# Optimization experiments

Measured on AMD Instinct MI355X. Metric: run time of the kernel, lower is better.

## Reference

```python
import jax, jax.numpy as jnp
import numpy as np

B, T, V, H = 4, 512, 8000, 7


def setup_inputs() -> dict:
    key = jax.random.key(0)
    k1, k2, k3 = jax.random.split(key, 3)
    return {
        "input_ids": jax.random.randint(k1, (B, T), 0, V),
        "frequencies": jax.random.normal(k2, (V,), dtype=jnp.float32) * 3.0,
        "amplitudes": 1.0 + jax.random.normal(k3, (V,), dtype=jnp.float32) * 0.1,
        "decay": jnp.asarray(1.5, dtype=jnp.float32),
        "chunk_size": 16,
    }


def reference(input_ids, frequencies, amplitudes, decay, chunk_size):
    h = jnp.arange(1, H + 1, dtype=frequencies.dtype)  # (H,)
    # harmonic expansion: freqs = f*[1..H], amps = A/[1..H]^decay
    all_f = frequencies[:, None] * h                    # (V, H)
    all_A = amplitudes[:, None] / h ** decay            # (V, H)
    seq_f = frequencies[input_ids][..., None] * h       # (B, T, H)
    seq_A = amplitudes[input_ids][..., None] / h ** decay

    nc = T // chunk_size
    sfc = seq_f.reshape(B, nc, chunk_size, H).transpose(1, 0, 2, 3)  # (nc,B,c,H)
    sAc = seq_A.reshape(B, nc, chunk_size, H).transpose(1, 0, 2, 3)

    def per_chunk(args):
        sf, sA = args  # (B,c,H)
        df = sf[:, :, :, None, None] - all_f[None, None, None, :, :]   # (B,c,H,V,H)
        amp = sA[:, :, :, None, None] * all_A[None, None, None, :, :]
        return 2.0 * (amp * jnp.sinc(2.0 * df)).sum(axis=(2, 4))       # (B,c,V)

    Cc = jax.lax.map(per_chunk, (sfc, sAc))            # (nc, B, c, V)
    C = Cc.transpose(1, 0, 2, 3).reshape(B, T, V)      # (B, T, V)

    cum = jnp.cumsum(C, axis=1)
    # logits[t] uses history 0..t-1 -> shift right by one, position 0 gets zeros
    logits = jnp.concatenate([jnp.zeros_like(cum[:, :1]), cum[:, :-1]], axis=1)
    return logits
```

## Files before the change

kernel.cpp:

```cpp
#include <hip/hip_runtime.h>
#include <math.h>


typedef float v2f __attribute__((ext_vector_type(2)));

constexpr int cB = 4, cT = 512, cV = 8000, cH = 7;
constexpr int GT = 4;
constexpr int NPLANE = 28;

__device__ __forceinline__ v2f pk_add(v2f a, v2f b) {
    v2f d; asm("v_pk_add_f32 %0, %1, %2" : "=v"(d) : "v"(a), "v"(b)); return d;
}
__device__ __forceinline__ v2f pk_mul(v2f a, v2f b) {
    v2f d; asm("v_pk_mul_f32 %0, %1, %2" : "=v"(d) : "v"(a), "v"(b)); return d;
}
__device__ __forceinline__ v2f pk_fma(v2f a, v2f b, v2f c) {
    v2f d; asm("v_pk_fma_f32 %0, %1, %2, %3" : "=v"(d) : "v"(a), "v"(b), "v"(c));
    return d;
}

__global__ __launch_bounds__(256) void wavelm_tab(
    const float* __restrict__ freq, const float* __restrict__ amp,
    const float* __restrict__ decay_p, float* __restrict__ tab)
{
    const int v = blockIdx.x * 256 + threadIdx.x;
    if (v >= cV) return;
    const float decay = decay_p[0];
    const float f = freq[v], A = amp[v];
    const float p2 = __builtin_amdgcn_exp2f(-decay);
    const float p3 = __builtin_amdgcn_exp2f(-decay * 1.5849625007f);
    const float p5 = __builtin_amdgcn_exp2f(-decay * 2.3219280949f);
    const float p7 = __builtin_amdgcn_exp2f(-decay * 2.8073549221f);
    const float rp[7] = {1.f, p2, p3, p2*p2, p5, p2*p3, p7};
    const float xr = f - rintf(f);
    const float s1 = __builtin_amdgcn_sinf(xr);
    const float c1 = __builtin_amdgcn_cosf(xr);
    float s = s1, c = c1;
#pragma unroll
    for (int k = 0; k < cH; ++k) {
        if (k) { const float sp = s, cp = c;
                 s = fmaf(sp, c1,  cp * s1);
                 c = fmaf(cp, c1, -(sp * s1)); }
        tab[(size_t)k * cV + v]        = s;
        tab[(size_t)(7 + k) * cV + v]  = c;
        tab[(size_t)(14 + k) * cV + v] = A * rp[k];
        tab[(size_t)(21 + k) * cV + v] = f * (float)(k + 1);
    }
}

__global__ __launch_bounds__(256) void wavelm_g(
    const int* __restrict__ ids, const float* __restrict__ tab,
    float* __restrict__ out)
{
    const int bt0 = blockIdx.y * GT;
    const int vh  = blockIdx.x * 256 + threadIdx.x;
    const bool valid = (vh * 2 < cV);
    const int vc = valid ? vh : 0;

    const v2f* tp = (const v2f*)tab;
    v2f nb[cH], sBw[cH], cBw[cH];
#pragma unroll
    for (int j = 0; j < cH; ++j) {
        const v2f s = tp[(size_t)j * (cV/2) + vc];
        const v2f c = tp[(size_t)(7 + j) * (cV/2) + vc];
        const v2f w = tp[(size_t)(14 + j) * (cV/2) + vc];
        const v2f a = tp[(size_t)(21 + j) * (cV/2) + vc];
        const v2f ws = w * 0.15915494309189535f;
        sBw[j] = s * ws;
        cBw[j] = c * ws;
        nb[j].x = -a.x;  nb[j].y = -a.y;
    }

    for (int g = 0; g < GT; ++g) {
        const int bt = bt0 + g;
        const int id = ids[bt];
        float sA[cH], cA[cH], wA[cH], aU[cH];
#pragma unroll
        for (int i = 0; i < cH; ++i) {
            sA[i] = tab[(size_t)i * cV + id];
            cA[i] = tab[(size_t)(7 + i) * cV + id];
            wA[i] = tab[(size_t)(14 + i) * cV + id];
            aU[i] = tab[(size_t)(21 + i) * cV + id];
        }

        float accx = 0.f, accy = 0.f;
        float mn = 3.0e38f, mx = 0.0f;
#pragma unroll
        for (int i = 0; i < cH; ++i) {
            v2f ai;  ai.x = aU[i];  ai.y = aU[i];
            v2f d[cH], p[cH];
#pragma unroll
            for (int j = 0; j < cH; ++j) d[j] = pk_add(ai, nb[j]);
            p[0] = d[0];
#pragma unroll
            for (int j = 1; j < cH; ++j) p[j] = pk_mul(p[j-1], d[j]);
            const float ptot = p[6].x * p[6].y;
            mn = fminf(mn, fminf(fabsf(p[6].x), fabsf(p[6].y)));
            mn = fminf(mn, fabsf(ptot));
            mx = fmaxf(mx, fabsf(ptot));
            const float rt = __builtin_amdgcn_rcpf(ptot);
            v2f r;  r.x = rt * p[6].y;  r.y = rt * p[6].x;
            v2f accS = (v2f)0.f, accC = (v2f)0.f;
#pragma unroll
            for (int j = cH - 1; j >= 1; --j) {
                const v2f inv = pk_mul(r, p[j-1]);
                accS = pk_fma(cBw[j], inv, accS);
                accC = pk_fma(sBw[j], inv, accC);
                r = pk_mul(r, d[j]);
            }
            accS = pk_fma(cBw[0], r, accS);
            accC = pk_fma(sBw[0], r, accC);
            const float tx = fmaf(sA[i], accS.x, -(cA[i] * accC.x));
            const float ty = fmaf(sA[i], accS.y, -(cA[i] * accC.y));
            accx = fmaf(wA[i], tx, accx);
            accy = fmaf(wA[i], ty, accy);
        }

        if (mn < 1e-37f || mx > 1e37f) {
            accx = 0.f;  accy = 0.f;
#pragma unroll
            for (int i = 0; i < cH; ++i) {
                float ax = 0.f, ay = 0.f;
#pragma unroll
                for (int j = 0; j < cH; ++j) {
                    const v2f w = tp[(size_t)(14 + j) * (cV/2) + vc];
                    const float dx = aU[i] + nb[j].x;
                    const float dy = aU[i] + nb[j].y;
                    const float snx = fmaf(sA[i], cBw[j].x, -(cA[i] * sBw[j].x));
                    const float sny = fmaf(sA[i], cBw[j].y, -(cA[i] * sBw[j].y));
                    float qx = snx * __builtin_amdgcn_rcpf(dx);
                    float qy = sny * __builtin_amdgcn_rcpf(dy);
                    qx = (dx == 0.f) ? w.x : qx;
                    qy = (dy == 0.f) ? w.y : qy;
                    ax += qx;  ay += qy;
                }
                accx = fmaf(wA[i], ax, accx);
                accy = fmaf(wA[i], ay, accy);
            }
        }

        if (valid) {
            v2f res;  res.x = 2.f * accx;  res.y = 2.f * accy;
            *(v2f*)(out + (size_t)bt * cV + (size_t)vh * 2) = res;
        }
    }
}

__global__ __launch_bounds__(256) void wavelm_seg(
    const float* __restrict__ out, float* __restrict__ segsum,
    int lgseg, int seglen)
{
    const int v = blockIdx.x * 256 + threadIdx.x;
    if (v >= cV) return;
    const int bs = blockIdx.y;
    const int b = bs >> lgseg, seg = bs & ((1 << lgseg) - 1);
    const float* p = out + ((size_t)b * cT + (size_t)seg * seglen) * cV + v;
    float a0 = 0.f, a1 = 0.f, a2 = 0.f, a3 = 0.f;
    for (int k = 0; k < seglen; k += 4) {
        a0 += p[(size_t)(k+0) * cV];
        a1 += p[(size_t)(k+1) * cV];
        a2 += p[(size_t)(k+2) * cV];
        a3 += p[(size_t)(k+3) * cV];
    }
    segsum[(size_t)bs * cV + v] = (a0 + a1) + (a2 + a3);
}

__global__ __launch_bounds__(256) void wavelm_scan2(
    float* __restrict__ out, const float* __restrict__ segsum,
    int lgseg, int seglen)
{
    const int v = blockIdx.x * 256 + threadIdx.x;
    if (v >= cV) return;
    const int bs = blockIdx.y;
    const int b = bs >> lgseg, seg = bs & ((1 << lgseg) - 1);
    const int nseg = 1 << lgseg;
    float base = 0.f;
    for (int sp = 0; sp < seg; ++sp)
        base += segsum[(size_t)(b * nseg + sp) * cV + v];
    float* p = out + ((size_t)b * cT + (size_t)seg * seglen) * cV + v;
    float acc = base;
#pragma unroll 8
    for (int k = 0; k < seglen; ++k) {
        const float c = p[(size_t)k * cV];
        p[(size_t)k * cV] = acc;
        acc += c;
    }
}

__global__ __launch_bounds__(256) void wavelm_scan(float* __restrict__ out)
{
    const int g = blockIdx.x * blockDim.x + threadIdx.x;
    if (g >= cB * cV) return;
    const int b = g / cV;
    const int v = g - b * cV;
    float* p = out + (size_t)b * cT * cV + v;
    float acc = 0.f;
#pragma unroll 8
    for (int t = 0; t < cT; ++t) {
        const float c = p[(size_t)t * cV];
        p[(size_t)t * cV] = acc;
        acc += c;
    }
}

extern "C" void kernel_launch(void* const* d_in, const int* in_sizes, int n_in,
                              void* d_out, int out_size, void* d_ws, size_t ws_size,
                              hipStream_t stream)
{
    const int*   ids  = (const int*)d_in[0];
    const float* freq = (const float*)d_in[1];
    const float* amp  = (const float*)d_in[2];
    const float* dec  = (const float*)d_in[3];
    float* out = (float*)d_out;
    float* tab = (float*)d_ws;
    float* segsum = tab + (size_t)NPLANE * cV;

    const size_t tab_b = (size_t)NPLANE * cV * sizeof(float);
    int lgseg = 4;
    while (lgseg > 0 &&
           tab_b + ((size_t)cB << lgseg) * cV * sizeof(float) > ws_size)
        --lgseg;
    const int use_seg =
        (lgseg > 0 &&
         tab_b + ((size_t)cB << lgseg) * cV * sizeof(float) <= ws_size) ? 1 : 0;

    wavelm_tab<<<(cV + 255) / 256, 256, 0, stream>>>(freq, amp, dec, tab);

    dim3 grid((cV / 2 + 255) / 256, cB * cT / GT);
    wavelm_g<<<grid, dim3(256), 0, stream>>>(ids, tab, out);

    if (use_seg) {
        const int nseg = 1 << lgseg;
        const int seglen = cT / nseg;
        dim3 sg((cV + 255) / 256, cB * nseg);
        wavelm_seg<<<sg, dim3(256), 0, stream>>>(out, segsum, lgseg, seglen);
        wavelm_scan2<<<sg, dim3(256), 0, stream>>>(out, segsum, lgseg, seglen);
    } else {
        const int nchains = cB * cV;
        wavelm_scan<<<(nchains + 255) / 256, dim3(256), 0, stream>>>(out);
    }
}
```

Baseline: 225.1 us.

## Fuse segment sums into main kernel and precompute packed per-token tables

The main kernel now sums its GT=8 output rows per column into a partial-sum buffer. A small scan over 64 segments and a short per-group rescan then replace the separate segment-sum pass that re-read the whole output. The table kernel also precomputes negated frequencies, scaled sin/cos terms and duplicated packed per-token values (including the 2x and sign folding), which cuts per-row loads and scalar ops in the inner loop. The fallback path now also triggers on non-finite accumulators. The cost is a larger workspace and a dependence on ws_size being big enough for the fast path.

```diff
diff --git a/kernel.cpp b/kernel.cpp
--- a/kernel.cpp
+++ b/kernel.cpp
@@ -5,8 +5,10 @@
 typedef float v2f __attribute__((ext_vector_type(2)));
 
 constexpr int cB = 4, cT = 512, cV = 8000, cH = 7;
-constexpr int GT = 4;
-constexpr int NPLANE = 28;
+constexpr int GT = 8;
+constexpr int NSEG = 64;
+constexpr int TABP  = 49;
+constexpr int TABUP = 21;
 
 __device__ __forceinline__ v2f pk_add(v2f a, v2f b) {
     v2f d; asm("v_pk_add_f32 %0, %1, %2" : "=v"(d) : "v"(a), "v"(b)); return d;
@@ -14,14 +16,17 @@
 __device__ __forceinline__ v2f pk_mul(v2f a, v2f b) {
     v2f d; asm("v_pk_mul_f32 %0, %1, %2" : "=v"(d) : "v"(a), "v"(b)); return d;
 }
-__device__ __forceinline__ v2f pk_fma(v2f a, v2f b, v2f c) {
-    v2f d; asm("v_pk_fma_f32 %0, %1, %2, %3" : "=v"(d) : "v"(a), "v"(b), "v"(c));
-    return d;
+__device__ __forceinline__ void pk_mul_ip(v2f& a, v2f b) {
+    asm("v_pk_mul_f32 %0, %0, %1" : "+v"(a) : "v"(b));
+}
+__device__ __forceinline__ void pk_acc(v2f& acc, v2f a, v2f b) {
+    asm("v_pk_fma_f32 %0, %1, %2, %0" : "+v"(acc) : "v"(a), "v"(b));
 }
 
 __global__ __launch_bounds__(256) void wavelm_tab(
     const float* __restrict__ freq, const float* __restrict__ amp,
-    const float* __restrict__ decay_p, float* __restrict__ tab)
+    const float* __restrict__ decay_p, float* __restrict__ tab,
+    v2f* __restrict__ tabU)
 {
     const int v = blockIdx.x * 256 + threadIdx.x;
     if (v >= cV) return;
@@ -32,6 +37,8 @@
     const float p5 = __builtin_amdgcn_exp2f(-decay * 2.3219280949f);
     const float p7 = __builtin_amdgcn_exp2f(-decay * 2.8073549221f);
     const float rp[7] = {1.f, p2, p3, p2*p2, p5, p2*p3, p7};
+    const float INV2PI = 0.15915494309189535f;
+
     const float xr = f - rintf(f);
     const float s1 = __builtin_amdgcn_sinf(xr);
     const float c1 = __builtin_amdgcn_cosf(xr);
@@ -41,16 +48,28 @@
         if (k) { const float sp = s, cp = c;
                  s = fmaf(sp, c1,  cp * s1);
                  c = fmaf(cp, c1, -(sp * s1)); }
+        const float w = A * rp[k];
+        const float b = f * (float)(k + 1);
         tab[(size_t)k * cV + v]        = s;
         tab[(size_t)(7 + k) * cV + v]  = c;
-        tab[(size_t)(14 + k) * cV + v] = A * rp[k];
-        tab[(size_t)(21 + k) * cV + v] = f * (float)(k + 1);
+        tab[(size_t)(14 + k) * cV + v] = w;
+        tab[(size_t)(21 + k) * cV + v] = b;
+        tab[(size_t)(28 + k) * cV + v] = -b;
+        tab[(size_t)(35 + k) * cV + v] = s * w * INV2PI;
+        tab[(size_t)(42 + k) * cV + v] = c * w * INV2PI;
+        v2f a2;  a2.x = b;             a2.y = b;
+        v2f s2;  s2.x = 2.f * w * s;   s2.y = s2.x;
+        v2f c2;  c2.x = -2.f * w * c;  c2.y = c2.x;
+        tabU[(size_t)k * cV + v]        = a2;
+        tabU[(size_t)(7 + k) * cV + v]  = s2;
+        tabU[(size_t)(14 + k) * cV + v] = c2;
     }
 }
 
 __global__ __launch_bounds__(256) void wavelm_g(
     const int* __restrict__ ids, const float* __restrict__ tab,
-    float* __restrict__ out)
+    const v2f* __restrict__ tabU, float* __restrict__ out,
+    float* __restrict__ part, int write_part)
 {
     const int bt0 = blockIdx.y * GT;
     const int vh  = blockIdx.x * 256 + threadIdx.x;
@@ -61,88 +80,125 @@
     v2f nb[cH], sBw[cH], cBw[cH];
 #pragma unroll
     for (int j = 0; j < cH; ++j) {
-        const v2f s = tp[(size_t)j * (cV/2) + vc];
-        const v2f c = tp[(size_t)(7 + j) * (cV/2) + vc];
-        const v2f w = tp[(size_t)(14 + j) * (cV/2) + vc];
-        const v2f a = tp[(size_t)(21 + j) * (cV/2) + vc];
-        const v2f ws = w * 0.15915494309189535f;
-        sBw[j] = s * ws;
-        cBw[j] = c * ws;
-        nb[j].x = -a.x;  nb[j].y = -a.y;
-    }
-
+        nb[j]  = tp[(size_t)(28 + j) * (cV/2) + vc];
+        sBw[j] = tp[(size_t)(35 + j) * (cV/2) + vc];
+        cBw[j] = tp[(size_t)(42 + j) * (cV/2) + vc];
+    }
+
+    v2f segacc = (v2f)0.f;
+#pragma unroll 1
     for (int g = 0; g < GT; ++g) {
         const int bt = bt0 + g;
         const int id = ids[bt];
-        float sA[cH], cA[cH], wA[cH], aU[cH];
+        const v2f* tu = tabU + id;
+
+        v2f accV = (v2f)0.f;
+        float mn = 3.0e38f, mx = 0.0f;
 #pragma unroll
         for (int i = 0; i < cH; ++i) {
-            sA[i] = tab[(size_t)i * cV + id];
-            cA[i] = tab[(size_t)(7 + i) * cV + id];
-            wA[i] = tab[(size_t)(14 + i) * cV + id];
-            aU[i] = tab[(size_t)(21 + i) * cV + id];
-        }
-
-        float accx = 0.f, accy = 0.f;
-        float mn = 3.0e38f, mx = 0.0f;
-#pragma unroll
-        for (int i = 0; i < cH; ++i) {
-            v2f ai;  ai.x = aU[i];  ai.y = aU[i];
+            const v2f aUv  = tu[(size_t)i * cV];
+            const v2f u2s  = tu[(size_t)(7 + i) * cV];
+            const v2f u2cn = tu[(size_t)(14 + i) * cV];
             v2f d[cH], p[cH];
 #pragma unroll
-            for (int j = 0; j < cH; ++j) d[j] = pk_add(ai, nb[j]);
+            for (int j = 0; j < cH; ++j) d[j] = pk_add(aUv, nb[j]);
             p[0] = d[0];
 #pragma unroll
             for (int j = 1; j < cH; ++j) p[j] = pk_mul(p[j-1], d[j]);
             const float ptot = p[6].x * p[6].y;
-            mn = fminf(mn, fminf(fabsf(p[6].x), fabsf(p[6].y)));
             mn = fminf(mn, fabsf(ptot));
             mx = fmaxf(mx, fabsf(ptot));
             const float rt = __builtin_amdgcn_rcpf(ptot);
             v2f r;  r.x = rt * p[6].y;  r.y = rt * p[6].x;
-            v2f accS = (v2f)0.f, accC = (v2f)0.f;
-#pragma unroll
-            for (int j = cH - 1; j >= 1; --j) {
-                const v2f inv = pk_mul(r, p[j-1]);
-                accS = pk_fma(cBw[j], inv, accS);
-                accC = pk_fma(sBw[j], inv, accC);
-                r = pk_mul(r, d[j]);
+            v2f inv = pk_mul(r, p[5]);
+            v2f accS = pk_mul(cBw[6], inv);
+            v2f accC = pk_mul(sBw[6], inv);
+            pk_mul_ip(r, d[6]);
+#pragma unroll
+            for (int j = 5; j >= 1; --j) {
+                inv = pk_mul(r, p[j-1]);
+                pk_acc(accS, cBw[j], inv);
+                pk_acc(accC, sBw[j], inv);
+                pk_mul_ip(r, d[j]);
             }
-            accS = pk_fma(cBw[0], r, accS);
-            accC = pk_fma(sBw[0], r, accC);
-            const float tx = fmaf(sA[i], accS.x, -(cA[i] * accC.x));
-            const float ty = fmaf(sA[i], accS.y, -(cA[i] * accC.y));
-            accx = fmaf(wA[i], tx, accx);
-            accy = fmaf(wA[i], ty, accy);
+            pk_acc(accS, cBw[0], r);
+            pk_acc(accC, sBw[0], r);
+            pk_acc(accV, u2s,  accS);
+            pk_acc(accV, u2cn, accC);
         }
 
-        if (mn < 1e-37f || mx > 1e37f) {
-            accx = 0.f;  accy = 0.f;
+        if (mn < 1e-37f || !(mx <= 1e37f) ||
+            !(fabsf(accV.x) + fabsf(accV.y) < 1e37f)) {
+            const float INV2PI = 0.15915494309189535f;
+            float ax = 0.f, ay = 0.f;
 #pragma unroll
             for (int i = 0; i < cH; ++i) {
-                float ax = 0.f, ay = 0.f;
+                const float sAi = tab[(size_t)i * cV + id];
+                const float cAi = tab[(size_t)(7 + i) * cV + id];
+                const float wAi = tab[(size_t)(14 + i) * cV + id];
+                const float aUi = tab[(size_t)(21 + i) * cV + id];
+                float rx = 0.f, ry = 0.f;
 #pragma unroll
                 for (int j = 0; j < cH; ++j) {
-                    const v2f w = tp[(size_t)(14 + j) * (cV/2) + vc];
-                    const float dx = aU[i] + nb[j].x;
-                    const float dy = aU[i] + nb[j].y;
-                    const float snx = fmaf(sA[i], cBw[j].x, -(cA[i] * sBw[j].x));
-                    const float sny = fmaf(sA[i], cBw[j].y, -(cA[i] * sBw[j].y));
-                    float qx = snx * __builtin_amdgcn_rcpf(dx);
-                    float qy = sny * __builtin_amdgcn_rcpf(dy);
-                    qx = (dx == 0.f) ? w.x : qx;
-                    qy = (dy == 0.f) ? w.y : qy;
-                    ax += qx;  ay += qy;
+                    const v2f sB = tp[(size_t)j * (cV/2) + vc];
+                    const v2f cB = tp[(size_t)(7 + j) * (cV/2) + vc];
+                    const v2f wB = tp[(size_t)(14 + j) * (cV/2) + vc];
+                    const v2f bb = tp[(size_t)(21 + j) * (cV/2) + vc];
+                    const float dx = aUi - bb.x;
+                    const float dy = aUi - bb.y;
+                    const float snx = fmaf(sAi, cB.x, -(cAi * sB.x));
+                    const float sny = fmaf(sAi, cB.y, -(cAi * sB.y));
+                    float qx = snx * INV2PI * __builtin_amdgcn_rcpf(dx);
+                    float qy = sny * INV2PI * __builtin_amdgcn_rcpf(dy);
+                    qx = (dx == 0.f) ? 1.f : qx;
+                    qy = (dy == 0.f) ? 1.f : qy;
+                    rx = fmaf(wB.x, qx, rx);
+                    ry = fmaf(wB.y, qy, ry);
                 }
-                accx = fmaf(wA[i], ax, accx);
-                accy = fmaf(wA[i], ay, accy);
+                ax = fmaf(2.f * wAi, rx, ax);
+                ay = fmaf(2.f * wAi, ry, ay);
             }
+            accV.x = ax;  accV.y = ay;
         }
 
-        if (valid) {
-            v2f res;  res.x = 2.f * accx;  res.y = 2.f * accy;
-            *(v2f*)(out + (size_t)bt * cV + (size_t)vh * 2) = res;
-        }
+        if (valid)
+            *(v2f*)(out + (size_t)bt * cV + (size_t)vh * 2) = accV;
+        segacc = pk_add(segacc, accV);
+    }
+
+    if (valid && write_part)
+        *(v2f*)(part + (size_t)blockIdx.y * cV + (size_t)vh * 2) = segacc;
+}
+
+__global__ __launch_bounds__(256) void wavelm_scanA(float* __restrict__ part)
+{
+    const int g = blockIdx.x * 256 + threadIdx.x;
+    if (g >= cB * cV) return;
+    const int b = g / cV;
+    const int v = g - b * cV;
+    float acc = 0.f;
+#pragma unroll 8
+    for (int s = 0; s < NSEG; ++s) {
+        const size_t idx = ((size_t)(b * NSEG + s)) * cV + v;
+        const float t = part[idx];
+        part[idx] = acc;
+        acc += t;
+    }
+}
+
+__global__ __launch_bounds__(256) void wavelm_scanB(
+    float* __restrict__ out, const float* __restrict__ part)
+{
+    const int v = blockIdx.x * 256 + threadIdx.x;
+    if (v >= cV) return;
+    const int grp = blockIdx.y;
+    float acc = part[(size_t)grp * cV + v];
+    float* p = out + (size_t)grp * GT * cV + v;
+#pragma unroll
+    for (int k = 0; k < GT; ++k) {
+        const float c = p[(size_t)k * cV];
+        p[(size_t)k * cV] = acc;
+        acc += c;
     }
 }
 
@@ -157,10 +213,8 @@
     const float* p = out + ((size_t)b * cT + (size_t)seg * seglen) * cV + v;
     float a0 = 0.f, a1 = 0.f, a2 = 0.f, a3 = 0.f;
     for (int k = 0; k < seglen; k += 4) {
-        a0 += p[(size_t)(k+0) * cV];
-        a1 += p[(size_t)(k+1) * cV];
-        a2 += p[(size_t)(k+2) * cV];
-        a3 += p[(size_t)(k+3) * cV];
+        a0 += p[(size_t)(k+0) * cV];  a1 += p[(size_t)(k+1) * cV];
+        a2 += p[(size_t)(k+2) * cV];  a3 += p[(size_t)(k+3) * cV];
     }
     segsum[(size_t)bs * cV + v] = (a0 + a1) + (a2 + a3);
 }
@@ -212,31 +266,40 @@
     const float* amp  = (const float*)d_in[2];
     const float* dec  = (const float*)d_in[3];
     float* out = (float*)d_out;
-    float* tab = (float*)d_ws;
-    float* segsum = tab + (size_t)NPLANE * cV;
-
-    const size_t tab_b = (size_t)NPLANE * cV * sizeof(float);
-    int lgseg = 4;
-    while (lgseg > 0 &&
-           tab_b + ((size_t)cB << lgseg) * cV * sizeof(float) > ws_size)
-        --lgseg;
-    const int use_seg =
-        (lgseg > 0 &&
-         tab_b + ((size_t)cB << lgseg) * cV * sizeof(float) <= ws_size) ? 1 : 0;
-
-    wavelm_tab<<<(cV + 255) / 256, 256, 0, stream>>>(freq, amp, dec, tab);
+
+    float* tab  = (float*)d_ws;
+    v2f*   tabU = (v2f*)(tab + (size_t)TABP * cV);
+    float* part = (float*)(tabU + (size_t)TABUP * cV);
+
+    const size_t tab_b  = (size_t)TABP * cV * sizeof(float);
+    const size_t tabu_b = (size_t)TABUP * cV * sizeof(v2f);
+    const size_t part_b = (size_t)cB * NSEG * cV * sizeof(float);
+    const int fast = (ws_size >= tab_b + tabu_b + part_b) ? 1 : 0;
+
+    wavelm_tab<<<(cV + 255) / 256, 256, 0, stream>>>(freq, amp, dec, tab, tabU);
 
     dim3 grid((cV / 2 + 255) / 256, cB * cT / GT);
-    wavelm_g<<<grid, dim3(256), 0, stream>>>(ids, tab, out);
-
-    if (use_seg) {
-        const int nseg = 1 << lgseg;
-        const int seglen = cT / nseg;
-        dim3 sg((cV + 255) / 256, cB * nseg);
-        wavelm_seg<<<sg, dim3(256), 0, stream>>>(out, segsum, lgseg, seglen);
-        wavelm_scan2<<<sg, dim3(256), 0, stream>>>(out, segsum, lgseg, seglen);
+    wavelm_g<<<grid, dim3(256), 0, stream>>>(ids, tab, tabU, out, part, fast);
+
+    if (fast) {
+        const int nchains = cB * cV;
+        wavelm_scanA<<<(nchains + 255) / 256, 256, 0, stream>>>(part);
+        dim3 sb((cV + 255) / 256, cB * NSEG);
+        wavelm_scanB<<<sb, dim3(256), 0, stream>>>(out, part);
     } else {
-        const int nchains = cB * cV;
-        wavelm_scan<<<(nchains + 255) / 256, dim3(256), 0, stream>>>(out);
-    }
-}
+        float* segsum = part;
+        int lgseg = 4;
+        while (lgseg > 0 &&
+               tab_b + tabu_b + ((size_t)cB << lgseg) * cV * sizeof(float) > ws_size)
+            --lgseg;
+        if (lgseg > 0) {
+            const int nseg = 1 << lgseg, seglen = cT / nseg;
+            dim3 sg((cV + 255) / 256, cB * nseg);
+            wavelm_seg<<<sg, dim3(256), 0, stream>>>(out, segsum, lgseg, seglen);
+            wavelm_scan2<<<sg, dim3(256), 0, stream>>>(out, segsum, lgseg, seglen);
+        } else {
+            const int nchains = cB * cV;
+            wavelm_scan<<<(nchains + 255) / 256, dim3(256), 0, stream>>>(out);
+        }
+    }
+}
```

New measurement: 256.4 us. 1.14x slower.
